# Kernel tuning notes

Measured on AMD Instinct MI355X. Metric: run time of the kernel, lower is better.

## Reference

```python
import jax, jax.numpy as jnp
import numpy as np
import math

H = 16          # num heads
D = 64          # head dim
MAX_POS = 512   # max_position_embeddings


def setup_inputs() -> dict:
    key = jax.random.key(0)
    ks = jax.random.split(key, 8)
    B, S, E = 8, 512, 1024
    scale = 1.0 / math.sqrt(E)
    return {
        "hidden_states": jax.random.normal(ks[0], (B, S, E), jnp.float32),
        "attention_mask": jnp.zeros((B, 1, 1, S), jnp.float32),
        "Wq": jax.random.normal(ks[1], (E, E), jnp.float32) * scale,
        "bq": jnp.zeros((E,), jnp.float32),
        "Wk": jax.random.normal(ks[2], (E, E), jnp.float32) * scale,
        "bk": jnp.zeros((E,), jnp.float32),
        "Wv": jax.random.normal(ks[3], (E, E), jnp.float32) * scale,
        "bv": jnp.zeros((E,), jnp.float32),
        "dist_emb": jax.random.normal(ks[4], (2 * MAX_POS - 1, D), jnp.float32) * 0.02,
    }


def reference(hidden_states, attention_mask, Wq, bq, Wk, bk, Wv, bv, dist_emb):
    B, S, E = hidden_states.shape

    def heads(x):  # [B,S,E] -> [B,H,S,D]
        return x.reshape(B, S, H, D).transpose(0, 2, 1, 3)

    q = heads(hidden_states @ Wq + bq)
    k = heads(hidden_states @ Wk + bk)
    v = heads(hidden_states @ Wv + bv)

    # raw scores [B,H,S,S]
    scores = jnp.einsum('bhld,bhrd->bhlr', q, k)

    # relative position embedding lookup: distance[l,r] = l - r
    pos = jnp.arange(S)
    distance = pos[:, None] - pos[None, :]               # [S,S]
    pe = dist_emb[distance + MAX_POS - 1]                # [S,S,D]
    scores = scores + jnp.einsum('bhld,lrd->bhlr', q, pe)
    scores = scores + jnp.einsum('bhrd,lrd->bhlr', k, pe)

    scores = scores / math.sqrt(D) + attention_mask
    probs = jax.nn.softmax(scores, axis=-1)

    ctx = jnp.einsum('bhlr,bhrd->bhld', probs, v)        # [B,H,S,D]
    ctx = ctx.transpose(0, 2, 1, 3).reshape(B, S, H * D)
    return ctx
```

## Files before the change

kernel.cpp:

```cpp
#include <hip/hip_runtime.h>

#define BATCH 8
#define SEQ   512
#define EMB   1024
#define NH    16
#define HD    64

typedef __bf16 bf16x8 __attribute__((ext_vector_type(8)));
typedef float  f32x4  __attribute__((ext_vector_type(4)));

__device__ __forceinline__ unsigned short f2bf(float f){
  union { float f; unsigned u; } v; v.f = f;
  unsigned r = v.u + 0x7FFFu + ((v.u >> 16) & 1u);
  return (unsigned short)(r >> 16);
}
__device__ __forceinline__ unsigned short f2bfr(float f){
  union { float f; unsigned u; } v; v.f = f;
  return (unsigned short)((v.u + 0x8000u) >> 16);
}
__device__ __forceinline__ float bf2f(unsigned short s){
  union { unsigned u; float f; } v; v.u = ((unsigned)s) << 16;
  return v.f;
}

__device__ __forceinline__ float dpp_max16(float x){
  int t;
  t = __builtin_amdgcn_update_dpp(0, __builtin_bit_cast(int, x), 0xB1, 0xF, 0xF, true);
  x = fmaxf(x, __builtin_bit_cast(float, t));
  t = __builtin_amdgcn_update_dpp(0, __builtin_bit_cast(int, x), 0x4E, 0xF, 0xF, true);
  x = fmaxf(x, __builtin_bit_cast(float, t));
  t = __builtin_amdgcn_update_dpp(0, __builtin_bit_cast(int, x), 0x141, 0xF, 0xF, true);
  x = fmaxf(x, __builtin_bit_cast(float, t));
  t = __builtin_amdgcn_update_dpp(0, __builtin_bit_cast(int, x), 0x140, 0xF, 0xF, true);
  x = fmaxf(x, __builtin_bit_cast(float, t));
  return x;
}
__device__ __forceinline__ float dpp_sum16(float x){
  int t;
  t = __builtin_amdgcn_update_dpp(0, __builtin_bit_cast(int, x), 0xB1, 0xF, 0xF, true);
  x += __builtin_bit_cast(float, t);
  t = __builtin_amdgcn_update_dpp(0, __builtin_bit_cast(int, x), 0x4E, 0xF, 0xF, true);
  x += __builtin_bit_cast(float, t);
  t = __builtin_amdgcn_update_dpp(0, __builtin_bit_cast(int, x), 0x141, 0xF, 0xF, true);
  x += __builtin_bit_cast(float, t);
  t = __builtin_amdgcn_update_dpp(0, __builtin_bit_cast(int, x), 0x140, 0xF, 0xF, true);
  x += __builtin_bit_cast(float, t);
  return x;
}

__device__ __forceinline__ int swzc(int row, int chunk){
  return row * 128 + (((chunk ^ (row & 7)) & 7) << 4);
}
__device__ __forceinline__ int swz2(int row, int col){
  return row * 128 + ((((col >> 3) ^ (row & 7)) & 7) << 4) + ((col & 7) << 1);
}

__device__ __forceinline__ void gload16(const unsigned short* g, unsigned char* lds){
  __builtin_amdgcn_global_load_lds((const __attribute__((address_space(1))) unsigned int*)g,
                                   (__attribute__((address_space(3))) unsigned int*)lds,
                                   16, 0, 0);
}

__device__ __forceinline__ void bar_lds(){
  asm volatile("s_waitcnt lgkmcnt(0)" ::: "memory");
  __builtin_amdgcn_s_barrier();
}

__global__ void k_prep(const float* __restrict__ hid, unsigned short* __restrict__ hidb,
                       const float* __restrict__ dist, unsigned short* __restrict__ distb){
  int bid = blockIdx.x;
  if (bid < 4096){
    int i = (bid * 256 + threadIdx.x) * 4;
    float4 v = *(const float4*)(hid + i);
    ushort4 o; o.x = f2bf(v.x); o.y = f2bf(v.y); o.z = f2bf(v.z); o.w = f2bf(v.w);
    *(ushort4*)(hidb + i) = o;
  } else {
    int i = (bid - 4096) * 256 + threadIdx.x;
    distb[i] = (i < 1023 * 64) ? f2bf(dist[i]) : (unsigned short)0;
  }
}

__global__ void k_wt3(const float* __restrict__ Wq, const float* __restrict__ Wk,
                      const float* __restrict__ Wv, unsigned short* __restrict__ wqt,
                      unsigned short* __restrict__ wkt, unsigned short* __restrict__ wvt){
  const float* W = (blockIdx.z == 0) ? Wq : (blockIdx.z == 1) ? Wk : Wv;
  unsigned short* WT = (blockIdx.z == 0) ? wqt : (blockIdx.z == 1) ? wkt : wvt;
  __shared__ float t[32][33];
  int n0 = blockIdx.x * 32, k0 = blockIdx.y * 32;
  int tx = threadIdx.x, ty = threadIdx.y;
#pragma unroll
  for (int i = 0; i < 4; i++)
    t[ty + 8*i][tx] = W[(k0 + ty + 8*i) * EMB + n0 + tx];
  __syncthreads();
#pragma unroll
  for (int i = 0; i < 4; i++)
    WT[(n0 + ty + 8*i) * EMB + k0 + tx] = f2bf(t[tx][ty + 8*i]);
}

__global__ __launch_bounds__(256, 3) void k_gemm3(const unsigned short* __restrict__ A,
                                                  const unsigned short* __restrict__ wqt,
                                                  const unsigned short* __restrict__ wkt,
                                                  const unsigned short* __restrict__ wvt,
                                                  const float* __restrict__ bq,
                                                  const float* __restrict__ bk,
                                                  const float* __restrict__ bv,
                                                  unsigned short* __restrict__ qb,
                                                  unsigned short* __restrict__ kb,
                                                  unsigned short* __restrict__ vtb){
  int z = blockIdx.z;
  const unsigned short* BT = (z == 0) ? wqt : (z == 1) ? wkt : wvt;
  const float* bias = (z == 0) ? bq : (z == 1) ? bk : bv;
  unsigned short* out = (z == 0) ? qb : (z == 1) ? kb : vtb;
  int mode = (z == 2);

  __shared__ __align__(16) unsigned char sA[128 * 128];
  __shared__ __align__(16) unsigned char sB[128 * 128];
  int m0 = blockIdx.y * 128, n0 = blockIdx.x * 128;
  int t = threadIdx.x, w = t >> 6, lane = t & 63, g = lane >> 4, lr = lane & 15;
  int rowbase = (w >> 1) * 64, colbase = (w & 1) * 64;
  int lrow = lane >> 3, lc = lane & 7;
  f32x4 acc[4][4] = {};
  for (int k0 = 0; k0 < EMB; k0 += 64){
    __syncthreads();
#pragma unroll
    for (int i = 0; i < 4; i++){
      int row = (w + 4*i) * 8 + lrow;
      int cg  = lc ^ (row & 7);
      gload16(A  + (m0 + row) * EMB + k0 + cg*8, sA + (w + 4*i) * 1024);
      gload16(BT + (n0 + row) * EMB + k0 + cg*8, sB + (w + 4*i) * 1024);
    }
    __syncthreads();
#pragma unroll
    for (int kk = 0; kk < 2; kk++){
      bf16x8 af[4], bfv[4];
#pragma unroll
      for (int i = 0; i < 4; i++) af[i]  = *(const bf16x8*)(sA + swzc(rowbase + 16*i + lr, kk*4 + g));
#pragma unroll
      for (int j = 0; j < 4; j++) bfv[j] = *(const bf16x8*)(sB + swzc(colbase + 16*j + lr, kk*4 + g));
#pragma unroll
      for (int i = 0; i < 4; i++)
#pragma unroll
        for (int j = 0; j < 4; j++)
          acc[i][j] = __builtin_amdgcn_mfma_f32_16x16x32_bf16(af[i], bfv[j], acc[i][j], 0, 0, 0);
    }
  }
#pragma unroll
  for (int i = 0; i < 4; i++)
#pragma unroll
    for (int j = 0; j < 4; j++)
#pragma unroll
      for (int r = 0; r < 4; r++){
        int m = m0 + rowbase + 16*i + 4*g + r;
        int n = n0 + colbase + 16*j + lr;
        float val = acc[i][j][r] + bias[n];
        int b = m >> 9, s = m & 511, h = n >> 6, d = n & 63;
        int idx = (mode == 0) ? (((b*NH + h)*SEQ + s)*HD + d)
                              : (((b*NH + h)*HD + d)*SEQ + s);
        out[idx] = f2bf(val);
      }
}

__global__ __launch_bounds__(256, 2) void k_attn(const unsigned short* __restrict__ qb,
                                                 const unsigned short* __restrict__ kb,
                                                 const unsigned short* __restrict__ vtb,
                                                 const unsigned short* __restrict__ distb,
                                                 const float* __restrict__ mask,
                                                 float* __restrict__ out){
  __shared__ __align__(16) unsigned char sK[64 * 128];
  __shared__ __align__(16) unsigned char sV[64 * 128];
  __shared__ __align__(16) unsigned char sSA[4][2624];
  __shared__ __align__(16) unsigned char sSB[4][2560];

  const float SCL  = 0.125f * 1.4426950408889634f;
  const float L2E  = 1.4426950408889634f;

  int bid = blockIdx.x;
  int wgid = (bid & 7) * 128 + (bid >> 3);
  int lt = wgid & 7, h = (wgid >> 3) & 15, b = wgid >> 7;
  int L0 = lt * 64;
  int bh = b * NH + h;
  int t = threadIdx.x, w = t >> 6, lane = t & 63, g = lane >> 4, lr = lane & 15;
  int lbase = 16 * w;
  unsigned char* mySA = sSA[w];
  unsigned char* mySB = sSB[w];
  unsigned char* myP  = mySA;
  const float* maskp = mask + b * SEQ;

  const unsigned short* qrow = qb + (bh * SEQ + L0 + lbase + lr) * HD + 8 * g;
  bf16x8 aq0 = *(const bf16x8*)qrow;
  bf16x8 aq1 = *(const bf16x8*)(qrow + 32);

  bf16x8 pe[5][2];
#define LOAD_PE(JB) do {                                                     \
    const unsigned short* _pb = distb + ((JB) + 16*w + lr) * HD + 8*g;       \
    _Pragma("unroll")                                                        \
    for (int _j = 0; _j < 5; _j++){                                          \
      pe[_j][0] = *(const bf16x8*)(_pb + _j*16*HD);                          \
      pe[_j][1] = *(const bf16x8*)(_pb + _j*16*HD + 32); }                   \
  } while(0)

  int lrow = lane >> 3, lc = lane & 7;
  int row0 = w * 8 + lrow,      row1 = (w + 4) * 8 + lrow;
  int cg0  = lc ^ (row0 & 7),   cg1  = lc ^ (row1 & 7);
  const unsigned short* kbase = kb  + bh * SEQ * HD;
  const unsigned short* vbase = vtb + bh * HD * SEQ;

  uint4 kst0 = *(const uint4*)(kbase + row0 * HD  + cg0 * 8);
  uint4 kst1 = *(const uint4*)(kbase + row1 * HD  + cg1 * 8);
  uint4 vst0 = *(const uint4*)(vbase + row0 * SEQ + cg0 * 8);
  uint4 vst1 = *(const uint4*)(vbase + row1 * SEQ + cg1 * 8);
  LOAD_PE(L0 + 448);

  f32x4 o[4] = {};
  float mrun[4], srun[4];
#pragma unroll
  for (int r = 0; r < 4; r++){ mrun[r] = -1e30f; srun[r] = 0.f; }

  for (int rt = 0; rt < 8; rt++){
    int R0 = rt * 64;

    bar_lds();

    *(uint4*)(sK + w * 1024 + lane * 16)       = kst0;
    *(uint4*)(sK + (w + 4) * 1024 + lane * 16) = kst1;
    *(uint4*)(sV + w * 1024 + lane * 16)       = vst0;
    *(uint4*)(sV + (w + 4) * 1024 + lane * 16) = vst1;

    if (rt < 7){
      const unsigned short* ks = kbase + (R0 + 64) * HD;
      const unsigned short* vs = vbase + (R0 + 64);
      kst0 = *(const uint4*)(ks + row0 * HD  + cg0 * 8);
      kst1 = *(const uint4*)(ks + row1 * HD  + cg1 * 8);
      vst0 = *(const uint4*)(vs + row0 * SEQ + cg0 * 8);
      vst1 = *(const uint4*)(vs + row1 * SEQ + cg1 * 8);
    }

    bar_lds();

    float mreg[4];
#pragma unroll
    for (int f = 0; f < 4; f++) mreg[f] = maskp[R0 + 16*f + lr];

    __builtin_amdgcn_s_setprio(1);
    f32x4 sc[4];
#pragma unroll
    for (int f = 0; f < 4; f++){
      bf16x8 k0 = *(const bf16x8*)(sK + swzc(16*f + lr, g));
      bf16x8 k1 = *(const bf16x8*)(sK + swzc(16*f + lr, 4 + g));
      f32x4 a = {};
      a = __builtin_amdgcn_mfma_f32_16x16x32_bf16(aq0, k0, a, 0, 0, 0);
      a = __builtin_amdgcn_mfma_f32_16x16x32_bf16(aq1, k1, a, 0, 0, 0);
      sc[f] = a;
      f32x4 b0 = {}, b1 = {};
      b0 = __builtin_amdgcn_mfma_f32_16x16x32_bf16(k0, pe[3 - f][0], b0, 0, 0, 0);
      b0 = __builtin_amdgcn_mfma_f32_16x16x32_bf16(k1, pe[3 - f][1], b0, 0, 0, 0);
      b1 = __builtin_amdgcn_mfma_f32_16x16x32_bf16(k0, pe[4 - f][0], b1, 0, 0, 0);
      b1 = __builtin_amdgcn_mfma_f32_16x16x32_bf16(k1, pe[4 - f][1], b1, 0, 0, 0);
#pragma unroll
      for (int reg = 0; reg < 4; reg++){
        int ss = 4*g + reg + lr;
        float v = (ss >= 15) ? b0[reg] : b1[reg];
        int row = 16*f + 4*g + reg;
        int col = (ss + 1) & 15;
        *(unsigned short*)(mySB + row*40 + col*2) = f2bfr(v);
      }
    }

#pragma unroll
    for (int jt2 = 0; jt2 < 5; jt2++){
      f32x4 a = {};
      a = __builtin_amdgcn_mfma_f32_16x16x32_bf16(aq0, pe[jt2][0], a, 0, 0, 0);
      a = __builtin_amdgcn_mfma_f32_16x16x32_bf16(aq1, pe[jt2][1], a, 0, 0, 0);
#pragma unroll
      for (int reg = 0; reg < 4; reg++){
        int rloc = 63 + 4*g + reg - lr - 16*jt2;
        int addr = ((unsigned)rloc < 64u) ? (rloc*40 + (4*g + reg)*2) : 2560;
        *(unsigned short*)(mySA + addr) = f2bfr(a[reg]);
      }
    }
    __builtin_amdgcn_s_setprio(0);

    if (rt < 7) LOAD_PE(L0 + 448 - 64*(rt + 1));

#pragma unroll
    for (int f = 0; f < 4; f++){
      ushort4 sa = *(const ushort4*)(mySA + (16*f + lr)*40 + 8*g);
      ushort4 sb = *(const ushort4*)(mySB + (16*f + lr)*40 + 8*g);
      float madd = mreg[f] * L2E;
      sc[f][0] = (sc[f][0] + bf2f(sa.x) + bf2f(sb.x)) * SCL + madd;
      sc[f][1] = (sc[f][1] + bf2f(sa.y) + bf2f(sb.y)) * SCL + madd;
      sc[f][2] = (sc[f][2] + bf2f(sa.z) + bf2f(sb.z)) * SCL + madd;
      sc[f][3] = (sc[f][3] + bf2f(sa.w) + bf2f(sb.w)) * SCL + madd;
    }

    float fac[4];
#pragma unroll
    for (int r = 0; r < 4; r++){
      float tm = fmaxf(fmaxf(sc[0][r], sc[1][r]), fmaxf(sc[2][r], sc[3][r]));
      tm = dpp_max16(tm);
      float mnew = fmaxf(mrun[r], tm);
      float fr = exp2f(mrun[r] - mnew);
      float ps = 0.f;
#pragma unroll
      for (int f = 0; f < 4; f++){ float p = exp2f(sc[f][r] - mnew); sc[f][r] = p; ps += p; }
      ps = dpp_sum16(ps);
      srun[r] = srun[r] * fr + ps;
      mrun[r] = mnew;
      fac[r]  = fr;
    }
#pragma unroll
    for (int df = 0; df < 4; df++)
#pragma unroll
      for (int r = 0; r < 4; r++) o[df][r] *= fac[r];

#pragma unroll
    for (int f = 0; f < 4; f++)
#pragma unroll
      for (int r = 0; r < 4; r++)
        *(unsigned short*)(myP + swz2(4*g + r, 16*f + lr)) = f2bfr(sc[f][r]);

    __builtin_amdgcn_s_setprio(1);
#pragma unroll
    for (int kk = 0; kk < 2; kk++){
      bf16x8 pf = *(const bf16x8*)(myP + swzc(lr, kk*4 + g));
#pragma unroll
      for (int df = 0; df < 4; df++){
        bf16x8 vf = *(const bf16x8*)(sV + swzc(16*df + lr, kk*4 + g));
        o[df] = __builtin_amdgcn_mfma_f32_16x16x32_bf16(pf, vf, o[df], 0, 0, 0);
      }
    }
    __builtin_amdgcn_s_setprio(0);
  }

#pragma unroll
  for (int r = 0; r < 4; r++){
    float inv = 1.0f / srun[r];
#pragma unroll
    for (int df = 0; df < 4; df++){
      int l = L0 + lbase + 4*g + r;
      out[(b * SEQ + l) * EMB + h * HD + 16*df + lr] = o[df][r] * inv;
    }
  }
#undef LOAD_PE
}

extern "C" void kernel_launch(void* const* d_in, const int* in_sizes, int n_in,
                              void* d_out, int out_size, void* d_ws, size_t ws_size,
                              hipStream_t stream) {
  (void)in_sizes; (void)n_in; (void)out_size; (void)ws_size;
  const float* hid  = (const float*)d_in[0];
  const float* mask = (const float*)d_in[1];
  const float* Wq   = (const float*)d_in[2];
  const float* bq   = (const float*)d_in[3];
  const float* Wk   = (const float*)d_in[4];
  const float* bk   = (const float*)d_in[5];
  const float* Wv   = (const float*)d_in[6];
  const float* bv   = (const float*)d_in[7];
  const float* dist = (const float*)d_in[8];
  float* out = (float*)d_out;

  unsigned char* ws = (unsigned char*)d_ws;
  unsigned short* hidb  = (unsigned short*)ws;
  unsigned short* wqt   = hidb + 4096 * 1024;
  unsigned short* wkt   = wqt  + 1024 * 1024;
  unsigned short* wvt   = wkt  + 1024 * 1024;
  unsigned short* distb = wvt  + 1024 * 1024;
  unsigned short* qb    = distb + 1024 * 64;
  unsigned short* kb    = qb + BATCH * NH * SEQ * HD;
  unsigned short* vtb   = kb + BATCH * NH * SEQ * HD;

  k_prep<<<4352, 256, 0, stream>>>(hid, hidb, dist, distb);
  k_wt3<<<dim3(32, 32, 3), dim3(32, 8), 0, stream>>>(Wq, Wk, Wv, wqt, wkt, wvt);
  k_gemm3<<<dim3(8, 32, 3), 256, 0, stream>>>(hidb, wqt, wkt, wvt, bq, bk, bv, qb, kb, vtb);
  k_attn<<<1024, 256, 0, stream>>>(qb, kb, vtb, distb, mask, out);
}
```

Measured before the change: 104.3 us.

## Merge prep kernels, hoist Q·PE MFMAs before barrier, add lazy softmax rescale

The bf16 conversion and weight-transpose kernels are merged into one launch, which removes a kernel boundary. In the attention loop, the Q·PE MFMA block and the mask load now run before the K/V LDS barrier, so they overlap with barrier waiting. Online softmax skips the max update and the output rescale when the running max grows by at most 8 in the log2 domain across the whole wavefront. This saves exp and multiply work but allows unnormalized values up to 2^8 and adds a wave-wide vote branch.

```diff
diff --git a/kernel.cpp b/kernel.cpp
--- a/kernel.cpp
+++ b/kernel.cpp
@@ -66,35 +66,37 @@
   __builtin_amdgcn_s_barrier();
 }
 
-__global__ void k_prep(const float* __restrict__ hid, unsigned short* __restrict__ hidb,
-                       const float* __restrict__ dist, unsigned short* __restrict__ distb){
+__global__ void k_pre(const float* __restrict__ hid, unsigned short* __restrict__ hidb,
+                      const float* __restrict__ dist, unsigned short* __restrict__ distb,
+                      const float* __restrict__ Wq, const float* __restrict__ Wk,
+                      const float* __restrict__ Wv, unsigned short* __restrict__ wqt,
+                      unsigned short* __restrict__ wkt, unsigned short* __restrict__ wvt){
   int bid = blockIdx.x;
+  int t = threadIdx.x;
   if (bid < 4096){
-    int i = (bid * 256 + threadIdx.x) * 4;
+    int i = (bid * 256 + t) * 4;
     float4 v = *(const float4*)(hid + i);
     ushort4 o; o.x = f2bf(v.x); o.y = f2bf(v.y); o.z = f2bf(v.z); o.w = f2bf(v.w);
     *(ushort4*)(hidb + i) = o;
+  } else if (bid < 4352){
+    int i = (bid - 4096) * 256 + t;
+    distb[i] = (i < 1023 * 64) ? f2bf(dist[i]) : (unsigned short)0;
   } else {
-    int i = (bid - 4096) * 256 + threadIdx.x;
-    distb[i] = (i < 1023 * 64) ? f2bf(dist[i]) : (unsigned short)0;
+    int wt = bid - 4352;
+    int z = wt >> 10, rem = wt & 1023;
+    const float* W = (z == 0) ? Wq : (z == 1) ? Wk : Wv;
+    unsigned short* WT = (z == 0) ? wqt : (z == 1) ? wkt : wvt;
+    __shared__ float tl[32][33];
+    int n0 = (rem & 31) * 32, k0 = (rem >> 5) * 32;
+    int tx = t & 31, ty = t >> 5;
+#pragma unroll
+    for (int i = 0; i < 4; i++)
+      tl[ty + 8*i][tx] = W[(k0 + ty + 8*i) * EMB + n0 + tx];
+    __syncthreads();
+#pragma unroll
+    for (int i = 0; i < 4; i++)
+      WT[(n0 + ty + 8*i) * EMB + k0 + tx] = f2bf(tl[tx][ty + 8*i]);
   }
-}
-
-__global__ void k_wt3(const float* __restrict__ Wq, const float* __restrict__ Wk,
-                      const float* __restrict__ Wv, unsigned short* __restrict__ wqt,
-                      unsigned short* __restrict__ wkt, unsigned short* __restrict__ wvt){
-  const float* W = (blockIdx.z == 0) ? Wq : (blockIdx.z == 1) ? Wk : Wv;
-  unsigned short* WT = (blockIdx.z == 0) ? wqt : (blockIdx.z == 1) ? wkt : wvt;
-  __shared__ float t[32][33];
-  int n0 = blockIdx.x * 32, k0 = blockIdx.y * 32;
-  int tx = threadIdx.x, ty = threadIdx.y;
-#pragma unroll
-  for (int i = 0; i < 4; i++)
-    t[ty + 8*i][tx] = W[(k0 + ty + 8*i) * EMB + n0 + tx];
-  __syncthreads();
-#pragma unroll
-  for (int i = 0; i < 4; i++)
-    WT[(n0 + ty + 8*i) * EMB + k0 + tx] = f2bf(t[tx][ty + 8*i]);
 }
 
 __global__ __launch_bounds__(256, 3) void k_gemm3(const unsigned short* __restrict__ A,
@@ -219,6 +221,25 @@
   for (int rt = 0; rt < 8; rt++){
     int R0 = rt * 64;
 
+    float mreg[4];
+#pragma unroll
+    for (int f = 0; f < 4; f++) mreg[f] = maskp[R0 + 16*f + lr];
+
+    __builtin_amdgcn_s_setprio(1);
+#pragma unroll
+    for (int jt2 = 0; jt2 < 5; jt2++){
+      f32x4 a = {};
+      a = __builtin_amdgcn_mfma_f32_16x16x32_bf16(aq0, pe[jt2][0], a, 0, 0, 0);
+      a = __builtin_amdgcn_mfma_f32_16x16x32_bf16(aq1, pe[jt2][1], a, 0, 0, 0);
+#pragma unroll
+      for (int reg = 0; reg < 4; reg++){
+        int rloc = 63 + 4*g + reg - lr - 16*jt2;
+        int addr = ((unsigned)rloc < 64u) ? (rloc*40 + (4*g + reg)*2) : 2560;
+        *(unsigned short*)(mySA + addr) = f2bfr(a[reg]);
+      }
+    }
+    __builtin_amdgcn_s_setprio(0);
+
     bar_lds();
 
     *(uint4*)(sK + w * 1024 + lane * 16)       = kst0;
@@ -236,10 +257,6 @@
     }
 
     bar_lds();
-
-    float mreg[4];
-#pragma unroll
-    for (int f = 0; f < 4; f++) mreg[f] = maskp[R0 + 16*f + lr];
 
     __builtin_amdgcn_s_setprio(1);
     f32x4 sc[4];
@@ -265,19 +282,6 @@
         *(unsigned short*)(mySB + row*40 + col*2) = f2bfr(v);
       }
     }
-
-#pragma unroll
-    for (int jt2 = 0; jt2 < 5; jt2++){
-      f32x4 a = {};
-      a = __builtin_amdgcn_mfma_f32_16x16x32_bf16(aq0, pe[jt2][0], a, 0, 0, 0);
-      a = __builtin_amdgcn_mfma_f32_16x16x32_bf16(aq1, pe[jt2][1], a, 0, 0, 0);
-#pragma unroll
-      for (int reg = 0; reg < 4; reg++){
-        int rloc = 63 + 4*g + reg - lr - 16*jt2;
-        int addr = ((unsigned)rloc < 64u) ? (rloc*40 + (4*g + reg)*2) : 2560;
-        *(unsigned short*)(mySA + addr) = f2bfr(a[reg]);
-      }
-    }
     __builtin_amdgcn_s_setprio(0);
 
     if (rt < 7) LOAD_PE(L0 + 448 - 64*(rt + 1));
@@ -293,25 +297,38 @@
       sc[f][3] = (sc[f][3] + bf2f(sa.w) + bf2f(sb.w)) * SCL + madd;
     }
 
-    float fac[4];
+    float tm[4];
+    bool sml = true;
 #pragma unroll
     for (int r = 0; r < 4; r++){
-      float tm = fmaxf(fmaxf(sc[0][r], sc[1][r]), fmaxf(sc[2][r], sc[3][r]));
-      tm = dpp_max16(tm);
-      float mnew = fmaxf(mrun[r], tm);
-      float fr = exp2f(mrun[r] - mnew);
-      float ps = 0.f;
-#pragma unroll
-      for (int f = 0; f < 4; f++){ float p = exp2f(sc[f][r] - mnew); sc[f][r] = p; ps += p; }
-      ps = dpp_sum16(ps);
-      srun[r] = srun[r] * fr + ps;
-      mrun[r] = mnew;
-      fac[r]  = fr;
-    }
-#pragma unroll
-    for (int df = 0; df < 4; df++)
-#pragma unroll
-      for (int r = 0; r < 4; r++) o[df][r] *= fac[r];
+      float t0 = fmaxf(fmaxf(sc[0][r], sc[1][r]), fmaxf(sc[2][r], sc[3][r]));
+      tm[r] = dpp_max16(t0);
+      sml = sml && (tm[r] - mrun[r] <= 8.0f);
+    }
+    if (__all(sml)){
+#pragma unroll
+      for (int r = 0; r < 4; r++){
+        float ps = 0.f;
+#pragma unroll
+        for (int f = 0; f < 4; f++){ float p = exp2f(sc[f][r] - mrun[r]); sc[f][r] = p; ps += p; }
+        ps = dpp_sum16(ps);
+        srun[r] += ps;
+      }
+    } else {
+#pragma unroll
+      for (int r = 0; r < 4; r++){
+        float mnew = fmaxf(mrun[r], tm[r]);
+        float fr = exp2f(mrun[r] - mnew);
+        float ps = 0.f;
+#pragma unroll
+        for (int f = 0; f < 4; f++){ float p = exp2f(sc[f][r] - mnew); sc[f][r] = p; ps += p; }
+        ps = dpp_sum16(ps);
+        srun[r] = srun[r] * fr + ps;
+        mrun[r] = mnew;
+#pragma unroll
+        for (int df = 0; df < 4; df++) o[df][r] *= fr;
+      }
+    }
 
 #pragma unroll
     for (int f = 0; f < 4; f++)
@@ -369,8 +386,7 @@
   unsigned short* kb    = qb + BATCH * NH * SEQ * HD;
   unsigned short* vtb   = kb + BATCH * NH * SEQ * HD;
 
-  k_prep<<<4352, 256, 0, stream>>>(hid, hidb, dist, distb);
-  k_wt3<<<dim3(32, 32, 3), dim3(32, 8), 0, stream>>>(Wq, Wk, Wv, wqt, wkt, wvt);
+  k_pre<<<7424, 256, 0, stream>>>(hid, hidb, dist, distb, Wq, Wk, Wv, wqt, wkt, wvt);
   k_gemm3<<<dim3(8, 32, 3), 256, 0, stream>>>(hidb, wqt, wkt, wvt, bq, bk, bv, qb, kb, vtb);
   k_attn<<<1024, 256, 0, stream>>>(qb, kb, vtb, distb, mask, out);
 }
```

Result: slower. 110.4 us (+5.9%).
